# Optimization experiments

Measured on AMD Instinct MI355X. Metric: run time of the kernel, lower is better.

## Reference

```python
import jax, jax.numpy as jnp
import numpy as np

B, T, C = 2, 512, 128
H = 4 * C
EPS_LN = 1e-5
EPS_WKV = 1e-6


def setup_inputs() -> dict:
    key = jax.random.key(0)
    ks = jax.random.split(key, 12)
    def rn(i, shape, s):
        return jax.random.normal(ks[i], shape, jnp.float32) * s
    return {
        "x": jax.random.normal(ks[0], (B, T, C), jnp.float32),
        "ln1_g": jnp.ones((C,), jnp.float32), "ln1_b": jnp.zeros((C,), jnp.float32),
        "mu": rn(1, (C,), 0.1),
        "Wr": rn(2, (C, C), 0.02), "br": jnp.zeros((C,), jnp.float32),
        "Wk": rn(3, (C, C), 0.02), "bk": jnp.zeros((C,), jnp.float32),
        "Wv": rn(4, (C, C), 0.02), "bv": jnp.zeros((C,), jnp.float32),
        "w_decay": rn(5, (C,), 0.5),
        "Wo": rn(6, (C, C), 0.02), "bo": jnp.zeros((C,), jnp.float32),
        "ln2_g": jnp.ones((C,), jnp.float32), "ln2_b": jnp.zeros((C,), jnp.float32),
        "W1": rn(7, (C, H), 0.02), "b1": jnp.zeros((H,), jnp.float32),
        "W2": rn(8, (H, C), 0.02), "b2": jnp.zeros((C,), jnp.float32),
    }


def _ln(x, g, b):
    m = x.mean(-1, keepdims=True)
    v = ((x - m) ** 2).mean(-1, keepdims=True)
    return (x - m) * jax.lax.rsqrt(v + EPS_LN) * g + b


def _wkv_dir(k, v, w_lc):
    # k, v: (B,T,C); w_lc: (T,C) per-(position,channel) decay weight
    p = k[:, :, None, :] * w_lc[None, None, :, :]              # (B,T,L,C)
    p = jnp.exp(p - jax.lax.stop_gradient(p.max(-1, keepdims=True)))  # stable, max over C (as in source, dim=-1)
    p = p / (p.sum(-1, keepdims=True) + EPS_WKV)               # normalize over channel dim, as written in torch
    return jnp.einsum('btlc,blc->btc', p, v)


def _forward(x, ln1_g, ln1_b, mu, Wr, br, Wk, bk, Wv, bv, w_decay, Wo, bo, ln2_g, ln2_b, W1, b1, W2, b2):
    Tn = x.shape[1]
    h = _ln(x, ln1_g, ln1_b)
    # TemporalShift: past half shifted right, future half shifted left
    xp, xf = jnp.split(h, 2, axis=-1)
    xp = jnp.pad(xp, ((0, 0), (1, 0), (0, 0)))[:, :-1]
    xf = jnp.pad(xf, ((0, 0), (0, 1), (0, 0)))[:, 1:]
    hs = h + mu * jnp.concatenate([xp, xf], axis=-1)
    r = jax.nn.sigmoid(hs @ Wr + br)
    k = hs @ Wk + bk
    v = hs @ Wv + bv
    t = jnp.arange(Tn, dtype=x.dtype)[:, None]                 # (T,1)
    neg_w = -jnp.exp(w_decay)[None, :]                         # (1,C)
    w_f = neg_w * (Tn - 1 - t) / (Tn - 1)                      # (T,C)
    w_b = neg_w * t / (Tn - 1)                                 # (T,C)
    x_f = _wkv_dir(k, v, w_f)
    x_b = jnp.flip(_wkv_dir(jnp.flip(k, 1), jnp.flip(v, 1), w_b), 1)
    wk = r * (x_f + x_b) * 0.5
    y = x + wk @ Wo + bo
    h2 = _ln(y, ln2_g, ln2_b)
    m = jax.nn.gelu(h2 @ W1 + b1, approximate=False) @ W2 + b2
    return y + m


def reference(x, ln1_g, ln1_b, mu, Wr, br, Wk, bk, Wv, bv, w_decay, Wo, bo, ln2_g, ln2_b, W1, b1, W2, b2):
    return _forward(x, ln1_g, ln1_b, mu, Wr, br, Wk, bk, Wv, bv, w_decay, Wo, bo, ln2_g, ln2_b, W1, b1, W2, b2)
```

## Files before the change

kernel.cpp:

```cpp
#include <hip/hip_runtime.h>
#include <hip/hip_bf16.h>

#define Bq 2
#define Tq 512
#define Cq 128
#define Hq 512
#define NROW (Bq*Tq)

__device__ __forceinline__ float bfbits2f(unsigned short u) {
    return __uint_as_float(((unsigned)u) << 16);
}
__device__ __forceinline__ bool detect_f32(const void* sent) {
    return *(const unsigned*)sent == 0x3F800000u;
}
#define LD(p, i) (f32 ? ((const float*)(p))[i] : bfbits2f(((const unsigned short*)(p))[i]))
__device__ __forceinline__ float4 LD4(const void* p, int i, bool f32) {
    if (f32) return ((const float4*)p)[i >> 2];
    ushort4 u = *(const ushort4*)((const unsigned short*)p + i);
    return make_float4(bfbits2f(u.x), bfbits2f(u.y), bfbits2f(u.z), bfbits2f(u.w));
}

__global__ __launch_bounds__(512) void kA_qkv(
    const void* __restrict__ sent,
    const void* __restrict__ x,
    const void* __restrict__ ln1g, const void* __restrict__ ln1b,
    const void* __restrict__ mu,
    const void* __restrict__ Wr, const void* __restrict__ br,
    const void* __restrict__ Wk, const void* __restrict__ bk,
    const void* __restrict__ Wv, const void* __restrict__ bv,
    const void* __restrict__ wdec,
    float* __restrict__ r_out, float* __restrict__ u_out,
    float* __restrict__ v_out)
{
    const bool f32 = detect_f32(sent);
    int R0 = blockIdx.x * 2, tid = threadIdx.x;
    int g = tid >> 7, col = tid & 127;
    int t0 = R0 & (Tq - 1);
    int bbase = R0 - t0;

    __shared__ float h4[4][Cq];
    __shared__ __align__(16) float hsi[Cq][2];
    __shared__ float wred[8][2];

    {
        int t = t0 - 1 + g;
        int tcl = min(max(t, 0), Tq - 1);
        int row = bbase + tcl;
        float xv = LD(x, row * Cq + col);
        float s1 = xv, s2 = xv * xv;
        for (int off = 32; off; off >>= 1) {
            s1 += __shfl_xor(s1, off);
            s2 += __shfl_xor(s2, off);
        }
        int wid = tid >> 6;
        if ((tid & 63) == 0) { wred[wid][0] = s1; wred[wid][1] = s2; }
        __syncthreads();
        float S1 = wred[2 * g][0] + wred[2 * g + 1][0];
        float S2 = wred[2 * g][1] + wred[2 * g + 1][1];
        float m  = S1 * (1.f / Cq);
        float va = S2 * (1.f / Cq) - m * m;
        float rs = rsqrtf(va + 1e-5f);
        h4[g][col] = (xv - m) * rs * LD(ln1g, col) + LD(ln1b, col);
    }
    __syncthreads();

    if (g < 2) {
        int r2 = g, tt = t0 + r2;
        float hv = h4[r2 + 1][col];
        float nb;
        if (col < Cq / 2) nb = (tt > 0)      ? h4[r2][col]     : 0.f;
        else              nb = (tt < Tq - 1) ? h4[r2 + 2][col] : 0.f;
        hsi[col][r2] = hv + LD(mu, col) * nb;
    }
    __syncthreads();

    {
        int w = tid >> 6, lane = tid & 63;
        if (w < 6) {
            int m = w >> 1, r = w & 1;
            const void* W = (m == 0) ? Wr : (m == 1) ? Wk : Wv;
            int ks = lane >> 5, j0 = (lane & 31) * 4;
            float a0 = 0.f, a1 = 0.f, a2 = 0.f, a3 = 0.f;
            int cbase = ks * 64;
            for (int cc = cbase; cc < cbase + 64; cc += 4) {
                float4 w0 = LD4(W, (cc + 0) * Cq + j0, f32);
                float4 w1 = LD4(W, (cc + 1) * Cq + j0, f32);
                float4 w2 = LD4(W, (cc + 2) * Cq + j0, f32);
                float4 w3 = LD4(W, (cc + 3) * Cq + j0, f32);
                float h0 = hsi[cc + 0][r];
                float h1 = hsi[cc + 1][r];
                float h2 = hsi[cc + 2][r];
                float h3 = hsi[cc + 3][r];
                a0 += h0 * w0.x; a1 += h0 * w0.y; a2 += h0 * w0.z; a3 += h0 * w0.w;
                a0 += h1 * w1.x; a1 += h1 * w1.y; a2 += h1 * w1.z; a3 += h1 * w1.w;
                a0 += h2 * w2.x; a1 += h2 * w2.y; a2 += h2 * w2.z; a3 += h2 * w2.w;
                a0 += h3 * w3.x; a1 += h3 * w3.y; a2 += h3 * w3.z; a3 += h3 * w3.w;
            }
            a0 += __shfl_xor(a0, 32);
            a1 += __shfl_xor(a1, 32);
            a2 += __shfl_xor(a2, 32);
            a3 += __shfl_xor(a3, 32);
            if (ks == 0) {
                int row = R0 + r;
                if (m == 0) {
                    float4 bb = LD4(br, j0, f32);
                    float4 o;
                    o.x = 1.f / (1.f + __expf(-(a0 + bb.x)));
                    o.y = 1.f / (1.f + __expf(-(a1 + bb.y)));
                    o.z = 1.f / (1.f + __expf(-(a2 + bb.z)));
                    o.w = 1.f / (1.f + __expf(-(a3 + bb.w)));
                    *(float4*)&r_out[row * Cq + j0] = o;
                } else if (m == 1) {
                    float4 bb = LD4(bk, j0, f32);
                    float4 wd = LD4(wdec, j0, f32);
                    float4 o;
                    {
                        float w0c = fminf(fmaxf(wd.x, -20.f), 20.f);
                        float w1c = fminf(fmaxf(wd.y, -20.f), 20.f);
                        float w2c = fminf(fmaxf(wd.z, -20.f), 20.f);
                        float w3c = fminf(fmaxf(wd.w, -20.f), 20.f);
                        o.x = (a0 + bb.x) * (-__expf(w0c));
                        o.y = (a1 + bb.y) * (-__expf(w1c));
                        o.z = (a2 + bb.z) * (-__expf(w2c));
                        o.w = (a3 + bb.w) * (-__expf(w3c));
                        o.x = fminf(fmaxf(o.x, -30.f), 30.f);
                        o.y = fminf(fmaxf(o.y, -30.f), 30.f);
                        o.z = fminf(fmaxf(o.z, -30.f), 30.f);
                        o.w = fminf(fmaxf(o.w, -30.f), 30.f);
                    }
                    *(float4*)&u_out[row * Cq + j0] = o;
                } else {
                    float4 bb = LD4(bv, j0, f32);
                    float4 o = make_float4(a0 + bb.x, a1 + bb.y, a2 + bb.z, a3 + bb.w);
                    *(float4*)&v_out[row * Cq + j0] = o;
                }
            }
        }
    }
}

__global__ __launch_bounds__(512) void kB_wkv_ffn(
    const void* __restrict__ sent,
    const float* __restrict__ u_in,
    const float* __restrict__ v_in,
    const float* __restrict__ r_in,
    const void* __restrict__ x,
    const void* __restrict__ Wo, const void* __restrict__ bo,
    const void* __restrict__ lng, const void* __restrict__ lnb,
    const void* __restrict__ W1, const void* __restrict__ b1,
    const void* __restrict__ W2, const void* __restrict__ b2,
    void* __restrict__ out)
{
    const bool f32 = detect_f32(sent);
    int R0 = blockIdx.x * 2, tid = threadIdx.x;
    int b = R0 >> 9;
    const float inv511 = 1.f / (float)(Tq - 1);
    int w = tid >> 6, lane = tid & 63;

    __shared__ float u2[2][Cq];
    __shared__ __align__(16) float rinv2[Tq][2];
    __shared__ float part[8][2][Cq];
    __shared__ __align__(16) float wki[Cq][2];
    __shared__ __align__(16) float h2i[Cq][2];
    __shared__ __align__(16) float m1i[Hq][2];
    __shared__ __align__(16) float pbuf[16 * Cq * 2];
    __shared__ float wred[8][2];

    {
        const float4* us = (const float4*)(u_in + (size_t)R0 * Cq);
        ((float4*)u2)[lane] = us[lane];
    }
    float rv_pre = 0.f, xv_pre = 0.f;
    if (tid < 256) {
        int r = tid >> 7, c = tid & 127;
        rv_pre = r_in[(R0 + r) * Cq + c];
        xv_pre = LD(x, (R0 + r) * Cq + c);
    }

    {
        int l = (Tq - 1) - tid;
        float a = (float)tid * inv511 * 1.44269504f;
#pragma unroll
        for (int r = 0; r < 2; ++r) {
            float s0 = 0.f, s1 = 0.f, s2 = 0.f, s3 = 0.f;
            const float4* uu4 = (const float4*)u2[r];
            for (int cc = 0; cc < Cq / 4; ++cc) {
                float4 uv = uu4[cc];
                s0 += exp2f(a * uv.x);
                s1 += exp2f(a * uv.y);
                s2 += exp2f(a * uv.z);
                s3 += exp2f(a * uv.w);
            }
            rinv2[l][r] = 1.f / ((s0 + s1) + (s2 + s3) + 1e-6f);
        }
    }

    {
        int c2 = lane * 2;
        float u00 = u2[0][c2], u01 = u2[0][c2 + 1];
        float u10 = u2[1][c2], u11 = u2[1][c2 + 1];
        int j0 = w * 64;
        float jb = (float)j0;
        float e00 = __expf(u00 * jb * inv511), e01 = __expf(u01 * jb * inv511);
        float e10 = __expf(u10 * jb * inv511), e11 = __expf(u11 * jb * inv511);
        float g00 = __expf(u00 * inv511), g01 = __expf(u01 * inv511);
        float g10 = __expf(u10 * inv511), g11 = __expf(u11 * inv511);
        float a00 = 0.f, a01 = 0.f, a10 = 0.f, a11 = 0.f;
        int lhi = (Tq - 1) - j0;
        const float2* vp = (const float2*)(v_in + (size_t)b * Tq * Cq) + lane + (size_t)lhi * 64;
        const float2* rp = (const float2*)rinv2 + lhi;
        for (int it = 0; it < 16; ++it) {
            float2 v0 = vp[0];
            float2 v1 = vp[-64];
            float2 v2 = vp[-128];
            float2 v3 = vp[-192];
            float2 r0 = rp[0];
            float2 r1 = rp[-1];
            float2 r2 = rp[-2];
            float2 r3 = rp[-3];
            {
                float f1 = e00 * g00, f2 = f1 * g00, f3 = f2 * g00;
                a00 += v0.x * (e00 * r0.x);
                a00 += v1.x * (f1 * r1.x);
                a00 += v2.x * (f2 * r2.x);
                a00 += v3.x * (f3 * r3.x);
                e00 = f3 * g00;
            }
            {
                float f1 = e01 * g01, f2 = f1 * g01, f3 = f2 * g01;
                a01 += v0.y * (e01 * r0.x);
                a01 += v1.y * (f1 * r1.x);
                a01 += v2.y * (f2 * r2.x);
                a01 += v3.y * (f3 * r3.x);
                e01 = f3 * g01;
            }
            {
                float f1 = e10 * g10, f2 = f1 * g10, f3 = f2 * g10;
                a10 += v0.x * (e10 * r0.y);
                a10 += v1.x * (f1 * r1.y);
                a10 += v2.x * (f2 * r2.y);
                a10 += v3.x * (f3 * r3.y);
                e10 = f3 * g10;
            }
            {
                float f1 = e11 * g11, f2 = f1 * g11, f3 = f2 * g11;
                a11 += v0.y * (e11 * r0.y);
                a11 += v1.y * (f1 * r1.y);
                a11 += v2.y * (f2 * r2.y);
                a11 += v3.y * (f3 * r3.y);
                e11 = f3 * g11;
            }
            vp -= 256;
            rp -= 4;
        }
        part[w][0][c2]     = a00;
        part[w][0][c2 + 1] = a01;
        part[w][1][c2]     = a10;
        part[w][1][c2 + 1] = a11;
    }
    __syncthreads();

    if (tid < 256) {
        int r = tid >> 7, c = tid & 127;
        float acc = ((part[0][r][c] + part[1][r][c]) + (part[2][r][c] + part[3][r][c]))
                  + ((part[4][r][c] + part[5][r][c]) + (part[6][r][c] + part[7][r][c]));
        wki[c][r] = rv_pre * acc;
    }
    __syncthreads();

    {
        int ks = tid >> 5, c0 = (tid & 31) * 4;
        float a00 = 0.f, a01 = 0.f, a02 = 0.f, a03 = 0.f;
        float a10 = 0.f, a11 = 0.f, a12 = 0.f, a13 = 0.f;
        int k0 = ks * 8;
#pragma unroll
        for (int cc = k0; cc < k0 + 8; ++cc) {
            float4 wv   = LD4(Wo, cc * Cq + c0, f32);
            float2 wk2 = *(const float2*)&wki[cc][0];
            a00 += wk2.x * wv.x; a01 += wk2.x * wv.y; a02 += wk2.x * wv.z; a03 += wk2.x * wv.w;
            a10 += wk2.y * wv.x; a11 += wk2.y * wv.y; a12 += wk2.y * wv.z; a13 += wk2.y * wv.w;
        }
        *(float4*)&pbuf[(ks * Cq + c0) * 2]     = make_float4(a00, a10, a01, a11);
        *(float4*)&pbuf[(ks * Cq + c0 + 2) * 2] = make_float4(a02, a12, a03, a13);
    }
    __syncthreads();

    float yv = 0.f;
    if (tid < 256) {
        int c = tid & 127;
        float s = 0.f;
#pragma unroll
        for (int ks = 0; ks < 16; ++ks) s += pbuf[(ks * Cq + c) * 2 + (tid >> 7)];
        yv = xv_pre + s + LD(bo, c);
    }
    {
        float s1 = yv, s2 = yv * yv;
        for (int off = 32; off; off >>= 1) {
            s1 += __shfl_xor(s1, off);
            s2 += __shfl_xor(s2, off);
        }
        int wid = tid >> 6;
        if ((tid & 63) == 0) { wred[wid][0] = s1; wred[wid][1] = s2; }
        __syncthreads();
        if (tid < 256) {
            int r = tid >> 7, c = tid & 127;
            float S1 = wred[2 * r][0] + wred[2 * r + 1][0];
            float S2 = wred[2 * r][1] + wred[2 * r + 1][1];
            float m  = S1 * (1.f / Cq);
            float va = S2 * (1.f / Cq) - m * m;
            float rs = rsqrtf(va + 1e-5f);
            h2i[c][r] = (yv - m) * rs * LD(lng, c) + LD(lnb, c);
        }
    }
    __syncthreads();

    {
        int ks = tid >> 7, j0 = (tid & 127) * 4;
        float a00 = 0.f, a01 = 0.f, a02 = 0.f, a03 = 0.f;
        float a10 = 0.f, a11 = 0.f, a12 = 0.f, a13 = 0.f;
        int c0 = ks * 32;
#pragma unroll 4
        for (int cc = c0; cc < c0 + 32; ++cc) {
            float4 wv = LD4(W1, cc * Hq + j0, f32);
            float2 hv = *(const float2*)&h2i[cc][0];
            a00 += hv.x * wv.x; a01 += hv.x * wv.y; a02 += hv.x * wv.z; a03 += hv.x * wv.w;
            a10 += hv.y * wv.x; a11 += hv.y * wv.y; a12 += hv.y * wv.z; a13 += hv.y * wv.w;
        }
        *(float4*)&pbuf[(ks * Hq + j0) * 2]     = make_float4(a00, a10, a01, a11);
        *(float4*)&pbuf[(ks * Hq + j0 + 2) * 2] = make_float4(a02, a12, a03, a13);
    }
    __syncthreads();
    {
        int j = tid;
        float bb = LD(b1, j);
        float x0 = ((pbuf[(0 * Hq + j) * 2]     + pbuf[(1 * Hq + j) * 2])
                  + (pbuf[(2 * Hq + j) * 2]     + pbuf[(3 * Hq + j) * 2])) + bb;
        float x1 = ((pbuf[(0 * Hq + j) * 2 + 1] + pbuf[(1 * Hq + j) * 2 + 1])
                  + (pbuf[(2 * Hq + j) * 2 + 1] + pbuf[(3 * Hq + j) * 2 + 1])) + bb;
        m1i[j][0] = 0.5f * x0 * (1.f + erff(x0 * 0.70710678f));
        m1i[j][1] = 0.5f * x1 * (1.f + erff(x1 * 0.70710678f));
    }
    __syncthreads();

    {
        int ks = tid >> 5, c0 = (tid & 31) * 4;
        float a00 = 0.f, a01 = 0.f, a02 = 0.f, a03 = 0.f;
        float a10 = 0.f, a11 = 0.f, a12 = 0.f, a13 = 0.f;
        int h0 = ks * 32;
#pragma unroll 4
        for (int hh = h0; hh < h0 + 32; ++hh) {
            float4 wv = LD4(W2, hh * Cq + c0, f32);
            float2 mv = *(const float2*)&m1i[hh][0];
            a00 += mv.x * wv.x; a01 += mv.x * wv.y; a02 += mv.x * wv.z; a03 += mv.x * wv.w;
            a10 += mv.y * wv.x; a11 += mv.y * wv.y; a12 += mv.y * wv.z; a13 += mv.y * wv.w;
        }
        __syncthreads();
        *(float4*)&pbuf[(ks * Cq + c0) * 2]     = make_float4(a00, a10, a01, a11);
        *(float4*)&pbuf[(ks * Cq + c0 + 2) * 2] = make_float4(a02, a12, a03, a13);
    }
    __syncthreads();
    if (tid < 256) {
        int r = tid >> 7, c = tid & 127;
        float s = 0.f;
#pragma unroll
        for (int ks = 0; ks < 16; ++ks) s += pbuf[(ks * Cq + c) * 2 + r];
        float val = yv + s + LD(b2, c);
        int idx = (R0 + r) * Cq + c;
        if (f32) ((float*)out)[idx] = val;
        else     ((__hip_bfloat16*)out)[idx] = __float2bfloat16(val);
    }
}

extern "C" void kernel_launch(void* const* d_in, const int* in_sizes, int n_in,
                              void* d_out, int out_size, void* d_ws, size_t ws_size,
                              hipStream_t stream)
{
    const void* x    = d_in[0];
    const void* ln1g = d_in[1];
    const void* ln1b = d_in[2];
    const void* mu   = d_in[3];
    const void* Wr   = d_in[4];
    const void* br   = d_in[5];
    const void* Wk   = d_in[6];
    const void* bk   = d_in[7];
    const void* Wv   = d_in[8];
    const void* bv   = d_in[9];
    const void* wdec = d_in[10];
    const void* Wo   = d_in[11];
    const void* bo   = d_in[12];
    const void* ln2g = d_in[13];
    const void* ln2b = d_in[14];
    const void* W1   = d_in[15];
    const void* b1   = d_in[16];
    const void* W2   = d_in[17];
    const void* b2   = d_in[18];

    float* ws = (float*)d_ws;
    float* u  = ws;
    float* r  = ws + 131072;
    float* v  = ws + 262144;

    kA_qkv<<<NROW / 2, 512, 0, stream>>>(ln1g, x, ln1g, ln1b, mu, Wr, br, Wk, bk, Wv, bv, wdec, r, u, v);
    kB_wkv_ffn<<<NROW / 2, 512, 0, stream>>>(ln1g, u, v, r, x, Wo, bo, ln2g, ln2b, W1, b1, W2, b2, d_out);
}
```

Baseline: 149.8 us.

## Process one row per block instead of two to double grid parallelism

Both kernels now handle a single row per block and launch NROW blocks instead of NROW/2. The QKV kernel splits the K dimension across both wave halves and reduces through shared memory. WKV accumulation uses two accumulators per channel to shorten dependency chains, and launch bounds now request higher occupancy. The aim is more parallelism and shorter per-block latency, at the price of weight reuse: each weight load now serves one row instead of two, doubling total weight traffic.

```diff
diff --git a/kernel.cpp b/kernel.cpp
--- a/kernel.cpp
+++ b/kernel.cpp
@@ -20,7 +20,7 @@
     return make_float4(bfbits2f(u.x), bfbits2f(u.y), bfbits2f(u.z), bfbits2f(u.w));
 }
 
-__global__ __launch_bounds__(512) void kA_qkv(
+__global__ __launch_bounds__(512, 8) void kA_qkv(
     const void* __restrict__ sent,
     const void* __restrict__ x,
     const void* __restrict__ ln1g, const void* __restrict__ ln1b,
@@ -33,20 +33,22 @@
     float* __restrict__ v_out)
 {
     const bool f32 = detect_f32(sent);
-    int R0 = blockIdx.x * 2, tid = threadIdx.x;
+    int R = blockIdx.x, tid = threadIdx.x;
     int g = tid >> 7, col = tid & 127;
-    int t0 = R0 & (Tq - 1);
-    int bbase = R0 - t0;
-
-    __shared__ float h4[4][Cq];
-    __shared__ __align__(16) float hsi[Cq][2];
+    int t = R & (Tq - 1);
+    int bbase = R - t;
+
+    __shared__ float h3[3][Cq];
+    __shared__ float hsi[Cq];
+    __shared__ float partA[6][Cq];
     __shared__ float wred[8][2];
 
-    {
-        int t = t0 - 1 + g;
-        int tcl = min(max(t, 0), Tq - 1);
-        int row = bbase + tcl;
-        float xv = LD(x, row * Cq + col);
+    float xv = 0.f;
+    if (g < 3) {
+        int tt = min(max(t - 1 + g, 0), Tq - 1);
+        xv = LD(x, (bbase + tt) * Cq + col);
+    }
+    {
         float s1 = xv, s2 = xv * xv;
         for (int off = 32; off; off >>= 1) {
             s1 += __shfl_xor(s1, off);
@@ -54,92 +56,73 @@
         }
         int wid = tid >> 6;
         if ((tid & 63) == 0) { wred[wid][0] = s1; wred[wid][1] = s2; }
-        __syncthreads();
+    }
+    __syncthreads();
+    if (g < 3) {
         float S1 = wred[2 * g][0] + wred[2 * g + 1][0];
         float S2 = wred[2 * g][1] + wred[2 * g + 1][1];
         float m  = S1 * (1.f / Cq);
         float va = S2 * (1.f / Cq) - m * m;
         float rs = rsqrtf(va + 1e-5f);
-        h4[g][col] = (xv - m) * rs * LD(ln1g, col) + LD(ln1b, col);
-    }
-    __syncthreads();
-
-    if (g < 2) {
-        int r2 = g, tt = t0 + r2;
-        float hv = h4[r2 + 1][col];
+        h3[g][col] = (xv - m) * rs * LD(ln1g, col) + LD(ln1b, col);
+    }
+    __syncthreads();
+    if (g == 0) {
+        float hv = h3[1][col];
         float nb;
-        if (col < Cq / 2) nb = (tt > 0)      ? h4[r2][col]     : 0.f;
-        else              nb = (tt < Tq - 1) ? h4[r2 + 2][col] : 0.f;
-        hsi[col][r2] = hv + LD(mu, col) * nb;
+        if (col < Cq / 2) nb = (t > 0)      ? h3[0][col] : 0.f;
+        else              nb = (t < Tq - 1) ? h3[2][col] : 0.f;
+        hsi[col] = hv + LD(mu, col) * nb;
     }
     __syncthreads();
 
     {
         int w = tid >> 6, lane = tid & 63;
         if (w < 6) {
-            int m = w >> 1, r = w & 1;
+            int m = w >> 1, kh = w & 1;
             const void* W = (m == 0) ? Wr : (m == 1) ? Wk : Wv;
-            int ks = lane >> 5, j0 = (lane & 31) * 4;
+            int ks2 = lane >> 5, j0 = (lane & 31) * 4;
+            int cbase = kh * 64 + ks2 * 32;
             float a0 = 0.f, a1 = 0.f, a2 = 0.f, a3 = 0.f;
-            int cbase = ks * 64;
-            for (int cc = cbase; cc < cbase + 64; cc += 4) {
+            for (int cc = cbase; cc < cbase + 32; cc += 4) {
                 float4 w0 = LD4(W, (cc + 0) * Cq + j0, f32);
                 float4 w1 = LD4(W, (cc + 1) * Cq + j0, f32);
                 float4 w2 = LD4(W, (cc + 2) * Cq + j0, f32);
                 float4 w3 = LD4(W, (cc + 3) * Cq + j0, f32);
-                float h0 = hsi[cc + 0][r];
-                float h1 = hsi[cc + 1][r];
-                float h2 = hsi[cc + 2][r];
-                float h3 = hsi[cc + 3][r];
+                float h0 = hsi[cc + 0], h1 = hsi[cc + 1];
+                float h2 = hsi[cc + 2], h3v = hsi[cc + 3];
                 a0 += h0 * w0.x; a1 += h0 * w0.y; a2 += h0 * w0.z; a3 += h0 * w0.w;
                 a0 += h1 * w1.x; a1 += h1 * w1.y; a2 += h1 * w1.z; a3 += h1 * w1.w;
                 a0 += h2 * w2.x; a1 += h2 * w2.y; a2 += h2 * w2.z; a3 += h2 * w2.w;
-                a0 += h3 * w3.x; a1 += h3 * w3.y; a2 += h3 * w3.z; a3 += h3 * w3.w;
+                a0 += h3v * w3.x; a1 += h3v * w3.y; a2 += h3v * w3.z; a3 += h3v * w3.w;
             }
             a0 += __shfl_xor(a0, 32);
             a1 += __shfl_xor(a1, 32);
             a2 += __shfl_xor(a2, 32);
             a3 += __shfl_xor(a3, 32);
-            if (ks == 0) {
-                int row = R0 + r;
-                if (m == 0) {
-                    float4 bb = LD4(br, j0, f32);
-                    float4 o;
-                    o.x = 1.f / (1.f + __expf(-(a0 + bb.x)));
-                    o.y = 1.f / (1.f + __expf(-(a1 + bb.y)));
-                    o.z = 1.f / (1.f + __expf(-(a2 + bb.z)));
-                    o.w = 1.f / (1.f + __expf(-(a3 + bb.w)));
-                    *(float4*)&r_out[row * Cq + j0] = o;
-                } else if (m == 1) {
-                    float4 bb = LD4(bk, j0, f32);
-                    float4 wd = LD4(wdec, j0, f32);
-                    float4 o;
-                    {
-                        float w0c = fminf(fmaxf(wd.x, -20.f), 20.f);
-                        float w1c = fminf(fmaxf(wd.y, -20.f), 20.f);
-                        float w2c = fminf(fmaxf(wd.z, -20.f), 20.f);
-                        float w3c = fminf(fmaxf(wd.w, -20.f), 20.f);
-                        o.x = (a0 + bb.x) * (-__expf(w0c));
-                        o.y = (a1 + bb.y) * (-__expf(w1c));
-                        o.z = (a2 + bb.z) * (-__expf(w2c));
-                        o.w = (a3 + bb.w) * (-__expf(w3c));
-                        o.x = fminf(fmaxf(o.x, -30.f), 30.f);
-                        o.y = fminf(fmaxf(o.y, -30.f), 30.f);
-                        o.z = fminf(fmaxf(o.z, -30.f), 30.f);
-                        o.w = fminf(fmaxf(o.w, -30.f), 30.f);
-                    }
-                    *(float4*)&u_out[row * Cq + j0] = o;
-                } else {
-                    float4 bb = LD4(bv, j0, f32);
-                    float4 o = make_float4(a0 + bb.x, a1 + bb.y, a2 + bb.z, a3 + bb.w);
-                    *(float4*)&v_out[row * Cq + j0] = o;
-                }
-            }
-        }
-    }
-}
-
-__global__ __launch_bounds__(512) void kB_wkv_ffn(
+            if (ks2 == 0) *(float4*)&partA[w][j0] = make_float4(a0, a1, a2, a3);
+        }
+    }
+    __syncthreads();
+
+    if (g < 3) {
+        int m = g;
+        float a = partA[2 * m][col] + partA[2 * m + 1][col];
+        if (m == 0) {
+            r_out[R * Cq + col] = 1.f / (1.f + __expf(-(a + LD(br, col))));
+        } else if (m == 1) {
+            float wd = LD(wdec, col);
+            wd = fminf(fmaxf(wd, -20.f), 20.f);
+            float uu = (a + LD(bk, col)) * (-__expf(wd));
+            uu = fminf(fmaxf(uu, -30.f), 30.f);
+            u_out[R * Cq + col] = uu;
+        } else {
+            v_out[R * Cq + col] = a + LD(bv, col);
+        }
+    }
+}
+
+__global__ __launch_bounds__(512, 8) void kB_wkv_ffn(
     const void* __restrict__ sent,
     const float* __restrict__ u_in,
     const float* __restrict__ v_in,
@@ -152,146 +135,108 @@
     void* __restrict__ out)
 {
     const bool f32 = detect_f32(sent);
-    int R0 = blockIdx.x * 2, tid = threadIdx.x;
-    int b = R0 >> 9;
+    int R = blockIdx.x, tid = threadIdx.x;
+    int b = R >> 9;
     const float inv511 = 1.f / (float)(Tq - 1);
     int w = tid >> 6, lane = tid & 63;
 
-    __shared__ float u2[2][Cq];
-    __shared__ __align__(16) float rinv2[Tq][2];
-    __shared__ float part[8][2][Cq];
-    __shared__ __align__(16) float wki[Cq][2];
-    __shared__ __align__(16) float h2i[Cq][2];
-    __shared__ __align__(16) float m1i[Hq][2];
-    __shared__ __align__(16) float pbuf[16 * Cq * 2];
-    __shared__ float wred[8][2];
-
-    {
-        const float4* us = (const float4*)(u_in + (size_t)R0 * Cq);
-        ((float4*)u2)[lane] = us[lane];
-    }
-    float rv_pre = 0.f, xv_pre = 0.f;
-    if (tid < 256) {
-        int r = tid >> 7, c = tid & 127;
-        rv_pre = r_in[(R0 + r) * Cq + c];
-        xv_pre = LD(x, (R0 + r) * Cq + c);
+    __shared__ float u1[Cq];
+    __shared__ float rinv1[Tq];
+    __shared__ float partB[8][Cq];
+    __shared__ float wk1[Cq];
+    __shared__ float h21[Cq];
+    __shared__ float m11[Hq];
+    __shared__ __align__(16) float pbuf[16 * Cq];
+    __shared__ float wred2[8][2];
+
+    {
+        const float2* us = (const float2*)(u_in + (size_t)R * Cq);
+        ((float2*)u1)[lane] = us[lane];
     }
 
     {
         int l = (Tq - 1) - tid;
-        float a = (float)tid * inv511 * 1.44269504f;
-#pragma unroll
-        for (int r = 0; r < 2; ++r) {
-            float s0 = 0.f, s1 = 0.f, s2 = 0.f, s3 = 0.f;
-            const float4* uu4 = (const float4*)u2[r];
-            for (int cc = 0; cc < Cq / 4; ++cc) {
-                float4 uv = uu4[cc];
-                s0 += exp2f(a * uv.x);
-                s1 += exp2f(a * uv.y);
-                s2 += exp2f(a * uv.z);
-                s3 += exp2f(a * uv.w);
-            }
-            rinv2[l][r] = 1.f / ((s0 + s1) + (s2 + s3) + 1e-6f);
-        }
+        float a = (float)tid * (inv511 * 1.44269504f);
+        float s0 = 0.f, s1 = 0.f, s2 = 0.f, s3 = 0.f;
+        const float4* uu4 = (const float4*)u1;
+        for (int cc = 0; cc < Cq / 4; ++cc) {
+            float4 uv = uu4[cc];
+            s0 += exp2f(a * uv.x);
+            s1 += exp2f(a * uv.y);
+            s2 += exp2f(a * uv.z);
+            s3 += exp2f(a * uv.w);
+        }
+        rinv1[l] = 1.f / ((s0 + s1) + (s2 + s3) + 1e-6f);
     }
 
     {
         int c2 = lane * 2;
-        float u00 = u2[0][c2], u01 = u2[0][c2 + 1];
-        float u10 = u2[1][c2], u11 = u2[1][c2 + 1];
+        float ux = u1[c2], uy = u1[c2 + 1];
         int j0 = w * 64;
         float jb = (float)j0;
-        float e00 = __expf(u00 * jb * inv511), e01 = __expf(u01 * jb * inv511);
-        float e10 = __expf(u10 * jb * inv511), e11 = __expf(u11 * jb * inv511);
-        float g00 = __expf(u00 * inv511), g01 = __expf(u01 * inv511);
-        float g10 = __expf(u10 * inv511), g11 = __expf(u11 * inv511);
-        float a00 = 0.f, a01 = 0.f, a10 = 0.f, a11 = 0.f;
+        float ex = __expf(ux * jb * inv511), ey = __expf(uy * jb * inv511);
+        float gx = __expf(ux * inv511),      gy = __expf(uy * inv511);
+        float ax = 0.f, ay = 0.f, bx = 0.f, by = 0.f;
         int lhi = (Tq - 1) - j0;
         const float2* vp = (const float2*)(v_in + (size_t)b * Tq * Cq) + lane + (size_t)lhi * 64;
-        const float2* rp = (const float2*)rinv2 + lhi;
+        const float* rp = rinv1 + lhi;
         for (int it = 0; it < 16; ++it) {
             float2 v0 = vp[0];
             float2 v1 = vp[-64];
             float2 v2 = vp[-128];
             float2 v3 = vp[-192];
-            float2 r0 = rp[0];
-            float2 r1 = rp[-1];
-            float2 r2 = rp[-2];
-            float2 r3 = rp[-3];
+            float r0 = rp[0], r1 = rp[-1], r2 = rp[-2], r3 = rp[-3];
             {
-                float f1 = e00 * g00, f2 = f1 * g00, f3 = f2 * g00;
-                a00 += v0.x * (e00 * r0.x);
-                a00 += v1.x * (f1 * r1.x);
-                a00 += v2.x * (f2 * r2.x);
-                a00 += v3.x * (f3 * r3.x);
-                e00 = f3 * g00;
+                float f1 = ex * gx, f2 = f1 * gx, f3 = f2 * gx;
+                ax += v0.x * (ex * r0);
+                bx += v1.x * (f1 * r1);
+                ax += v2.x * (f2 * r2);
+                bx += v3.x * (f3 * r3);
+                ex = f3 * gx;
             }
             {
-                float f1 = e01 * g01, f2 = f1 * g01, f3 = f2 * g01;
-                a01 += v0.y * (e01 * r0.x);
-                a01 += v1.y * (f1 * r1.x);
-                a01 += v2.y * (f2 * r2.x);
-                a01 += v3.y * (f3 * r3.x);
-                e01 = f3 * g01;
-            }
-            {
-                float f1 = e10 * g10, f2 = f1 * g10, f3 = f2 * g10;
-                a10 += v0.x * (e10 * r0.y);
-                a10 += v1.x * (f1 * r1.y);
-                a10 += v2.x * (f2 * r2.y);
-                a10 += v3.x * (f3 * r3.y);
-                e10 = f3 * g10;
-            }
-            {
-                float f1 = e11 * g11, f2 = f1 * g11, f3 = f2 * g11;
-                a11 += v0.y * (e11 * r0.y);
-                a11 += v1.y * (f1 * r1.y);
-                a11 += v2.y * (f2 * r2.y);
-                a11 += v3.y * (f3 * r3.y);
-                e11 = f3 * g11;
+                float f1 = ey * gy, f2 = f1 * gy, f3 = f2 * gy;
+                ay += v0.y * (ey * r0);
+                by += v1.y * (f1 * r1);
+                ay += v2.y * (f2 * r2);
+                by += v3.y * (f3 * r3);
+                ey = f3 * gy;
             }
             vp -= 256;
             rp -= 4;
         }
-        part[w][0][c2]     = a00;
-        part[w][0][c2 + 1] = a01;
-        part[w][1][c2]     = a10;
-        part[w][1][c2 + 1] = a11;
-    }
-    __syncthreads();
-
-    if (tid < 256) {
-        int r = tid >> 7, c = tid & 127;
-        float acc = ((part[0][r][c] + part[1][r][c]) + (part[2][r][c] + part[3][r][c]))
-                  + ((part[4][r][c] + part[5][r][c]) + (part[6][r][c] + part[7][r][c]));
-        wki[c][r] = rv_pre * acc;
+        partB[w][c2]     = ax + bx;
+        partB[w][c2 + 1] = ay + by;
+    }
+    __syncthreads();
+
+    if (tid < Cq) {
+        float acc = ((partB[0][tid] + partB[1][tid]) + (partB[2][tid] + partB[3][tid]))
+                  + ((partB[4][tid] + partB[5][tid]) + (partB[6][tid] + partB[7][tid]));
+        wk1[tid] = r_in[(size_t)R * Cq + tid] * acc;
     }
     __syncthreads();
 
     {
         int ks = tid >> 5, c0 = (tid & 31) * 4;
-        float a00 = 0.f, a01 = 0.f, a02 = 0.f, a03 = 0.f;
-        float a10 = 0.f, a11 = 0.f, a12 = 0.f, a13 = 0.f;
+        float a0 = 0.f, a1 = 0.f, a2 = 0.f, a3 = 0.f;
         int k0 = ks * 8;
 #pragma unroll
         for (int cc = k0; cc < k0 + 8; ++cc) {
-            float4 wv   = LD4(Wo, cc * Cq + c0, f32);
-            float2 wk2 = *(const float2*)&wki[cc][0];
-            a00 += wk2.x * wv.x; a01 += wk2.x * wv.y; a02 += wk2.x * wv.z; a03 += wk2.x * wv.w;
-            a10 += wk2.y * wv.x; a11 += wk2.y * wv.y; a12 += wk2.y * wv.z; a13 += wk2.y * wv.w;
-        }
-        *(float4*)&pbuf[(ks * Cq + c0) * 2]     = make_float4(a00, a10, a01, a11);
-        *(float4*)&pbuf[(ks * Cq + c0 + 2) * 2] = make_float4(a02, a12, a03, a13);
+            float4 wv = LD4(Wo, cc * Cq + c0, f32);
+            float wkv = wk1[cc];
+            a0 += wkv * wv.x; a1 += wkv * wv.y; a2 += wkv * wv.z; a3 += wkv * wv.w;
+        }
+        *(float4*)&pbuf[ks * Cq + c0] = make_float4(a0, a1, a2, a3);
     }
     __syncthreads();
 
     float yv = 0.f;
-    if (tid < 256) {
-        int c = tid & 127;
+    if (tid < Cq) {
         float s = 0.f;
 #pragma unroll
-        for (int ks = 0; ks < 16; ++ks) s += pbuf[(ks * Cq + c) * 2 + (tid >> 7)];
-        yv = xv_pre + s + LD(bo, c);
+        for (int ks = 0; ks < 16; ++ks) s += pbuf[ks * Cq + tid];
+        yv = LD(x, (size_t)R * Cq + tid) + s + LD(bo, tid);
     }
     {
         float s1 = yv, s2 = yv * yv;
@@ -300,72 +245,72 @@
             s2 += __shfl_xor(s2, off);
         }
         int wid = tid >> 6;
-        if ((tid & 63) == 0) { wred[wid][0] = s1; wred[wid][1] = s2; }
+        if ((tid & 63) == 0) { wred2[wid][0] = s1; wred2[wid][1] = s2; }
+    }
+    __syncthreads();
+    if (tid < Cq) {
+        float S1 = wred2[0][0] + wred2[1][0];
+        float S2 = wred2[0][1] + wred2[1][1];
+        float m  = S1 * (1.f / Cq);
+        float va = S2 * (1.f / Cq) - m * m;
+        float rs = rsqrtf(va + 1e-5f);
+        h21[tid] = (yv - m) * rs * LD(lng, tid) + LD(lnb, tid);
+    }
+    __syncthreads();
+
+    {
+        int ks = tid >> 7, j0 = (tid & 127) * 4;
+        float a0 = 0.f, a1 = 0.f, a2 = 0.f, a3 = 0.f;
+        int c0 = ks * 32;
+        for (int cc = c0; cc < c0 + 32; cc += 4) {
+            float4 w0 = LD4(W1, (cc + 0) * Hq + j0, f32);
+            float4 w1 = LD4(W1, (cc + 1) * Hq + j0, f32);
+            float4 w2 = LD4(W1, (cc + 2) * Hq + j0, f32);
+            float4 w3 = LD4(W1, (cc + 3) * Hq + j0, f32);
+            float h0 = h21[cc + 0], h1 = h21[cc + 1];
+            float h2 = h21[cc + 2], h3 = h21[cc + 3];
+            a0 += h0 * w0.x; a1 += h0 * w0.y; a2 += h0 * w0.z; a3 += h0 * w0.w;
+            a0 += h1 * w1.x; a1 += h1 * w1.y; a2 += h1 * w1.z; a3 += h1 * w1.w;
+            a0 += h2 * w2.x; a1 += h2 * w2.y; a2 += h2 * w2.z; a3 += h2 * w2.w;
+            a0 += h3 * w3.x; a1 += h3 * w3.y; a2 += h3 * w3.z; a3 += h3 * w3.w;
+        }
+        *(float4*)&pbuf[ks * Hq + j0] = make_float4(a0, a1, a2, a3);
+    }
+    __syncthreads();
+    {
+        int j = tid;
+        float xg = ((pbuf[0 * Hq + j] + pbuf[1 * Hq + j])
+                  + (pbuf[2 * Hq + j] + pbuf[3 * Hq + j])) + LD(b1, j);
+        m11[j] = 0.5f * xg * (1.f + erff(xg * 0.70710678f));
+    }
+    __syncthreads();
+
+    {
+        int ks = tid >> 5, c0 = (tid & 31) * 4;
+        float a0 = 0.f, a1 = 0.f, a2 = 0.f, a3 = 0.f;
+        int h0 = ks * 32;
+        for (int hh = h0; hh < h0 + 32; hh += 4) {
+            float4 w0 = LD4(W2, (hh + 0) * Cq + c0, f32);
+            float4 w1 = LD4(W2, (hh + 1) * Cq + c0, f32);
+            float4 w2 = LD4(W2, (hh + 2) * Cq + c0, f32);
+            float4 w3 = LD4(W2, (hh + 3) * Cq + c0, f32);
+            float m0 = m11[hh + 0], m1 = m11[hh + 1];
+            float m2 = m11[hh + 2], m3 = m11[hh + 3];
+            a0 += m0 * w0.x; a1 += m0 * w0.y; a2 += m0 * w0.z; a3 += m0 * w0.w;
+            a0 += m1 * w1.x; a1 += m1 * w1.y; a2 += m1 * w1.z; a3 += m1 * w1.w;
+            a0 += m2 * w2.x; a1 += m2 * w2.y; a2 += m2 * w2.z; a3 += m2 * w2.w;
+            a0 += m3 * w3.x; a1 += m3 * w3.y; a2 += m3 * w3.z; a3 += m3 * w3.w;
+        }
         __syncthreads();
-        if (tid < 256) {
-            int r = tid >> 7, c = tid & 127;
-            float S1 = wred[2 * r][0] + wred[2 * r + 1][0];
-            float S2 = wred[2 * r][1] + wred[2 * r + 1][1];
-            float m  = S1 * (1.f / Cq);
-            float va = S2 * (1.f / Cq) - m * m;
-            float rs = rsqrtf(va + 1e-5f);
-            h2i[c][r] = (yv - m) * rs * LD(lng, c) + LD(lnb, c);
-        }
-    }
-    __syncthreads();
-
-    {
-        int ks = tid >> 7, j0 = (tid & 127) * 4;
-        float a00 = 0.f, a01 = 0.f, a02 = 0.f, a03 = 0.f;
-        float a10 = 0.f, a11 = 0.f, a12 = 0.f, a13 = 0.f;
-        int c0 = ks * 32;
-#pragma unroll 4
-        for (int cc = c0; cc < c0 + 32; ++cc) {
-            float4 wv = LD4(W1, cc * Hq + j0, f32);
-            float2 hv = *(const float2*)&h2i[cc][0];
-            a00 += hv.x * wv.x; a01 += hv.x * wv.y; a02 += hv.x * wv.z; a03 += hv.x * wv.w;
-            a10 += hv.y * wv.x; a11 += hv.y * wv.y; a12 += hv.y * wv.z; a13 += hv.y * wv.w;
-        }
-        *(float4*)&pbuf[(ks * Hq + j0) * 2]     = make_float4(a00, a10, a01, a11);
-        *(float4*)&pbuf[(ks * Hq + j0 + 2) * 2] = make_float4(a02, a12, a03, a13);
-    }
-    __syncthreads();
-    {
-        int j = tid;
-        float bb = LD(b1, j);
-        float x0 = ((pbuf[(0 * Hq + j) * 2]     + pbuf[(1 * Hq + j) * 2])
-                  + (pbuf[(2 * Hq + j) * 2]     + pbuf[(3 * Hq + j) * 2])) + bb;
-        float x1 = ((pbuf[(0 * Hq + j) * 2 + 1] + pbuf[(1 * Hq + j) * 2 + 1])
-                  + (pbuf[(2 * Hq + j) * 2 + 1] + pbuf[(3 * Hq + j) * 2 + 1])) + bb;
-        m1i[j][0] = 0.5f * x0 * (1.f + erff(x0 * 0.70710678f));
-        m1i[j][1] = 0.5f * x1 * (1.f + erff(x1 * 0.70710678f));
-    }
-    __syncthreads();
-
-    {
-        int ks = tid >> 5, c0 = (tid & 31) * 4;
-        float a00 = 0.f, a01 = 0.f, a02 = 0.f, a03 = 0.f;
-        float a10 = 0.f, a11 = 0.f, a12 = 0.f, a13 = 0.f;
-        int h0 = ks * 32;
-#pragma unroll 4
-        for (int hh = h0; hh < h0 + 32; ++hh) {
-            float4 wv = LD4(W2, hh * Cq + c0, f32);
-            float2 mv = *(const float2*)&m1i[hh][0];
-            a00 += mv.x * wv.x; a01 += mv.x * wv.y; a02 += mv.x * wv.z; a03 += mv.x * wv.w;
-            a10 += mv.y * wv.x; a11 += mv.y * wv.y; a12 += mv.y * wv.z; a13 += mv.y * wv.w;
-        }
-        __syncthreads();
-        *(float4*)&pbuf[(ks * Cq + c0) * 2]     = make_float4(a00, a10, a01, a11);
-        *(float4*)&pbuf[(ks * Cq + c0 + 2) * 2] = make_float4(a02, a12, a03, a13);
-    }
-    __syncthreads();
-    if (tid < 256) {
-        int r = tid >> 7, c = tid & 127;
+        *(float4*)&pbuf[ks * Cq + c0] = make_float4(a0, a1, a2, a3);
+    }
+    __syncthreads();
+    if (tid < Cq) {
         float s = 0.f;
 #pragma unroll
-        for (int ks = 0; ks < 16; ++ks) s += pbuf[(ks * Cq + c) * 2 + r];
-        float val = yv + s + LD(b2, c);
-        int idx = (R0 + r) * Cq + c;
+        for (int ks = 0; ks < 16; ++ks) s += pbuf[ks * Cq + tid];
+        float val = yv + s + LD(b2, tid);
+        size_t idx = (size_t)R * Cq + tid;
         if (f32) ((float*)out)[idx] = val;
         else     ((__hip_bfloat16*)out)[idx] = __float2bfloat16(val);
     }
@@ -400,6 +345,6 @@
     float* r  = ws + 131072;
     float* v  = ws + 262144;
 
-    kA_qkv<<<NROW / 2, 512, 0, stream>>>(ln1g, x, ln1g, ln1b, mu, Wr, br, Wk, bk, Wv, bv, wdec, r, u, v);
-    kB_wkv_ffn<<<NROW / 2, 512, 0, stream>>>(ln1g, u, v, r, x, Wo, bo, ln2g, ln2b, W1, b1, W2, b2, d_out);
-}
+    kA_qkv<<<NROW, 512, 0, stream>>>(ln1g, x, ln1g, ln1b, mu, Wr, br, Wk, bk, Wv, bv, wdec, r, u, v);
+    kB_wkv_ffn<<<NROW, 512, 0, stream>>>(ln1g, u, v, r, x, Wo, bo, ln2g, ln2b, W1, b1, W2, b2, d_out);
+}
```

Result: slower. 381.8 us (+154.9%).
